# Kernel tuning notes

Hardware: AMD Instinct MI355X
Metric: run time of the kernel (lower is better)

Reference implementation:

```python
import jax, jax.numpy as jnp
import numpy as np

# ---- static module config (matches torch defaults) ----
N_LEVELS = 16
MIN_RES = 16
MAX_RES = 512
N_ENC = 2 ** 14
D = 3          # n_input_dims
E = 2          # n_embed_dims
B = 1 << 20    # number of query points

# per-level resolutions, computed in float32 to mirror torch's float32 log/exp
_gf = np.exp((np.log(np.float32(MAX_RES)) - np.log(np.float32(MIN_RES))) / np.float32(N_LEVELS - 1)).astype(np.float32)
RES = [int(np.floor(np.float32(MIN_RES) * _gf ** np.float32(l))) for l in range(N_LEVELS)]
DIRECT = [r ** D < N_ENC for r in RES]                  # small grids use direct ravel indexing
NLE = [min(r ** D, N_ENC) for r in RES]                  # encodings per level (sentinel row at index NLE[l])

# 2^D corner offsets, shape (8, 3)
OFFS = np.stack(np.meshgrid(*([np.arange(2)] * D), indexing='ij'), axis=-1).reshape(-1, D).astype(np.int32)
# instant-ngp spatial hashing primes
PRIMES = (1, 2654435761, 805459861)


def setup_inputs() -> dict:
    key = jax.random.key(0)
    k1, k2 = jax.random.split(key)
    x = jax.random.uniform(k1, (B, D), dtype=jnp.float32, minval=-1.0, maxval=1.0)
    # stacked per-level tables, padded to (N_ENC+1, E); rows >= NLE[l] zeroed
    emb = jax.random.uniform(k2, (N_LEVELS, N_ENC + 1, E), dtype=jnp.float32, minval=-1e-4, maxval=1e-4)
    row = np.arange(N_ENC + 1)
    valid = (row[None, :] < np.asarray(NLE)[:, None])    # (L, N_ENC+1); also zeroes the sentinel row
    emb = emb * jnp.asarray(valid[..., None], dtype=jnp.float32)
    return {"x": x, "emb": emb}


def _level_features(x, emb_l, R, n_encs, direct):
    offs = jnp.asarray(OFFS)                             # (8, 3)
    xs = (x + 1.0) * (R * 0.5) - 0.5                     # grid coords
    xl = jnp.floor(xs)
    frac = xs - xl                                       # (B, 3)
    xi = xl.astype(jnp.int32)
    c = xi[:, None, :] + offs[None, :, :]                # (B, 8, 3) corner indices
    # bilinear/trilinear weights: prod over dims of frac (offset=1) or 1-frac (offset=0)
    w = jnp.prod(jnp.where(offs[None].astype(bool), frac[:, None, :], 1.0 - frac[:, None, :]), axis=-1)  # (B, 8)
    w = jax.lax.stop_gradient(w)                         # torch computes weights under no_grad
    m = jnp.all((c >= 0) & (c < R), axis=-1)             # (B, 8) corner validity
    if direct:
        ids = (c[..., 0] * R + c[..., 1]) * R + c[..., 2]
    else:
        cu = c.astype(jnp.uint32)
        h = (cu[..., 0] * jnp.uint32(PRIMES[0])
             ^ cu[..., 1] * jnp.uint32(PRIMES[1])
             ^ cu[..., 2] * jnp.uint32(PRIMES[2]))
        ids = (h % jnp.uint32(n_encs)).astype(jnp.int32)
    ids = jnp.where(m, ids, n_encs)                      # invalid corners -> zero sentinel row
    return jnp.sum(emb_l[ids] * w[..., None], axis=1)    # (B, E)


def reference(x, emb):
    feats = [
        _level_features(x, emb[l], RES[l], NLE[l], DIRECT[l])
        for l in range(N_LEVELS)
    ]
    return jnp.stack(feats, axis=1)                      # (B, L, E)
```

## Files before the change

### kernel.cpp

```cpp
#include <hip/hip_runtime.h>


typedef __attribute__((ext_vector_type(2))) float f32x2;

#define B_POINTS (1 << 20)
#define N_LEVELS 16
#define TAB_F2   16385
#define WG       1024
#define NWG      512
#define NCHUNK   (NWG / N_LEVELS)
#define CHUNK    (B_POINTS / NCHUNK)
#define PPT      (CHUNK / WG)

__constant__ int   cRES[N_LEVELS]  = {16, 20, 25, 32, 40, 50, 64, 80,
                                      101, 128, 161, 203, 256, 322, 406, 512};
__constant__ float cHALF[N_LEVELS] = {8.f, 10.f, 12.5f, 16.f, 20.f, 25.f, 32.f, 40.f,
                                      50.5f, 64.f, 80.5f, 101.5f, 128.f, 161.f, 203.f, 256.f};

__global__ __launch_bounds__(WG)
void hashenc_lds(const float* __restrict__ x,
                 const float* __restrict__ emb,
                 float* __restrict__ out)
{
    __shared__ f32x2 tab[TAB_F2];

    const int bid = blockIdx.x;
    const int xcd = bid & 7;
    const int s   = bid >> 3;
    const int l   = s & 15;
    const int c   = ((s >> 4) << 3) | xcd;

    const int   R      = cRES[l];
    const float half   = cHALF[l];
    const bool  direct = (l < 3);

    const f32x2* __restrict__ gtab = (const f32x2*)emb + (size_t)l * TAB_F2;
    const int t = threadIdx.x;
#pragma unroll
    for (int j = 0; j < 16; ++j)
        tab[j * WG + t] = gtab[j * WG + t];
    if (t == 0) tab[16384] = gtab[16384];
    __syncthreads();

    const int base = c * CHUNK;
#pragma unroll 2
    for (int k = 0; k < PPT; ++k) {
        const int p = base + k * WG + t;

        const float x0 = x[p * 3 + 0];
        const float x1 = x[p * 3 + 1];
        const float x2 = x[p * 3 + 2];

        const float xs0 = (x0 + 1.0f) * half - 0.5f;
        const float xs1 = (x1 + 1.0f) * half - 0.5f;
        const float xs2 = (x2 + 1.0f) * half - 0.5f;
        const float fl0 = floorf(xs0), fl1 = floorf(xs1), fl2 = floorf(xs2);
        const float f0 = xs0 - fl0, f1 = xs1 - fl1, f2 = xs2 - fl2;
        const float g0 = 1.0f - f0, g1 = 1.0f - f1, g2 = 1.0f - f2;
        const int i0 = (int)fl0, i1 = (int)fl1, i2 = (int)fl2;

        const float wx0 = ((i0     >= 0) && (i0     < R)) ? g0 : 0.0f;
        const float wx1 = ((i0 + 1 >= 0) && (i0 + 1 < R)) ? f0 : 0.0f;
        const float wy0 = ((i1     >= 0) && (i1     < R)) ? g1 : 0.0f;
        const float wy1 = ((i1 + 1 >= 0) && (i1 + 1 < R)) ? f1 : 0.0f;
        const float wz0 = ((i2     >= 0) && (i2     < R)) ? g2 : 0.0f;
        const float wz1 = ((i2 + 1 >= 0) && (i2 + 1 < R)) ? f2 : 0.0f;

        const float pxy00 = wx0 * wy0, pxy01 = wx0 * wy1;
        const float pxy10 = wx1 * wy0, pxy11 = wx1 * wy1;
        const float w[8] = {pxy00 * wz0, pxy00 * wz1, pxy01 * wz0, pxy01 * wz1,
                            pxy10 * wz0, pxy10 * wz1, pxy11 * wz0, pxy11 * wz1};

        int id[8];
        if (direct) {
            const int Rm1 = R - 1;
            const int u0l = min(max(i0,     0), Rm1), u0h = min(max(i0 + 1, 0), Rm1);
            const int u1l = min(max(i1,     0), Rm1), u1h = min(max(i1 + 1, 0), Rm1);
            const int u2l = min(max(i2,     0), Rm1), u2h = min(max(i2 + 1, 0), Rm1);
            const int a0  = u0l * R, a1 = u0h * R;
            const int b00 = (a0 + u1l) * R, b01 = (a0 + u1h) * R;
            const int b10 = (a1 + u1l) * R, b11 = (a1 + u1h) * R;
            id[0] = b00 + u2l; id[1] = b00 + u2h; id[2] = b01 + u2l; id[3] = b01 + u2h;
            id[4] = b10 + u2l; id[5] = b10 + u2h; id[6] = b11 + u2l; id[7] = b11 + u2h;
        } else {
            const unsigned hx0 = (unsigned)i0,                   hx1 = (unsigned)(i0 + 1);
            const unsigned hy0 = (unsigned)i1 * 2654435761u,     hy1 = (unsigned)(i1 + 1) * 2654435761u;
            const unsigned hz0 = (unsigned)i2 * 805459861u,      hz1 = (unsigned)(i2 + 1) * 805459861u;
            id[0] = (int)((hx0 ^ hy0 ^ hz0) & 16383u); id[1] = (int)((hx0 ^ hy0 ^ hz1) & 16383u);
            id[2] = (int)((hx0 ^ hy1 ^ hz0) & 16383u); id[3] = (int)((hx0 ^ hy1 ^ hz1) & 16383u);
            id[4] = (int)((hx1 ^ hy0 ^ hz0) & 16383u); id[5] = (int)((hx1 ^ hy0 ^ hz1) & 16383u);
            id[6] = (int)((hx1 ^ hy1 ^ hz0) & 16383u); id[7] = (int)((hx1 ^ hy1 ^ hz1) & 16383u);
        }

        f32x2 acc = {0.0f, 0.0f};
#pragma unroll
        for (int q = 0; q < 8; ++q)
            acc += tab[id[q]] * w[q];

        ((f32x2*)out)[(size_t)p * N_LEVELS + l] = acc;
    }
}

extern "C" void kernel_launch(void* const* d_in, const int* in_sizes, int n_in,
                              void* d_out, int out_size, void* d_ws, size_t ws_size,
                              hipStream_t stream) {
    const float* x   = (const float*)d_in[0];
    const float* emb = (const float*)d_in[1];
    float* out = (float*)d_out;

    hashenc_lds<<<NWG, WG, 0, stream>>>(x, emb, out);
}
```

Baseline: 225.2 us.

## Prefetch point coordinates in groups and precompute byte offsets for LDS gathers

Halves the workgroup count so each block handles twice as many points per level. Coordinates for a group of four points are software-prefetched into registers, with the first group loaded before the table fill, which overlaps global loads with the LDS gathers. Address math is simplified: bounds checks are reduced to single comparisons, the scale uses a single FMA, and hash and direct indices are precomputed as byte offsets with the mask applied early. The trade-offs are fewer waves to hide latency, more register pressure, and a longer per-block tail.

```diff
diff --git a/kernel.cpp b/kernel.cpp
--- a/kernel.cpp
+++ b/kernel.cpp
@@ -7,10 +7,12 @@
 #define N_LEVELS 16
 #define TAB_F2   16385
 #define WG       1024
-#define NWG      512
+#define NWG      256
 #define NCHUNK   (NWG / N_LEVELS)
 #define CHUNK    (B_POINTS / NCHUNK)
 #define PPT      (CHUNK / WG)
+#define GRP      4
+#define NGRP     (PPT / GRP)
 
 __constant__ int   cRES[N_LEVELS]  = {16, 20, 25, 32, 40, 50, 64, 80,
                                       101, 128, 161, 203, 256, 322, 406, 512};
@@ -31,73 +33,105 @@
     const int c   = ((s >> 4) << 3) | xcd;
 
     const int   R      = cRES[l];
+    const int   Rm1    = R - 1;
     const float half   = cHALF[l];
+    const float hb     = half - 0.5f;
     const bool  direct = (l < 3);
+    const int   R8     = R * 8;
+    const int   RR8    = R * R * 8;
 
     const f32x2* __restrict__ gtab = (const f32x2*)emb + (size_t)l * TAB_F2;
-    const int t = threadIdx.x;
+    const int t    = threadIdx.x;
+    const int base = c * CHUNK + t;
+
+    float xa[GRP], xb[GRP], xcv[GRP];
+#pragma unroll
+    for (int j = 0; j < GRP; ++j) {
+        const int p = base + j * WG;
+        xa[j] = x[p * 3 + 0]; xb[j] = x[p * 3 + 1]; xcv[j] = x[p * 3 + 2];
+    }
+
 #pragma unroll
     for (int j = 0; j < 16; ++j)
         tab[j * WG + t] = gtab[j * WG + t];
     if (t == 0) tab[16384] = gtab[16384];
     __syncthreads();
 
-    const int base = c * CHUNK;
-#pragma unroll 2
-    for (int k = 0; k < PPT; ++k) {
-        const int p = base + k * WG + t;
+    const char* tb = (const char*)tab;
 
-        const float x0 = x[p * 3 + 0];
-        const float x1 = x[p * 3 + 1];
-        const float x2 = x[p * 3 + 2];
+    for (int kg = 0; kg < NGRP; ++kg) {
+        float ca[GRP], cb[GRP], cc[GRP];
+#pragma unroll
+        for (int j = 0; j < GRP; ++j) { ca[j] = xa[j]; cb[j] = xb[j]; cc[j] = xcv[j]; }
 
-        const float xs0 = (x0 + 1.0f) * half - 0.5f;
-        const float xs1 = (x1 + 1.0f) * half - 0.5f;
-        const float xs2 = (x2 + 1.0f) * half - 0.5f;
-        const float fl0 = floorf(xs0), fl1 = floorf(xs1), fl2 = floorf(xs2);
-        const float f0 = xs0 - fl0, f1 = xs1 - fl1, f2 = xs2 - fl2;
-        const float g0 = 1.0f - f0, g1 = 1.0f - f1, g2 = 1.0f - f2;
-        const int i0 = (int)fl0, i1 = (int)fl1, i2 = (int)fl2;
-
-        const float wx0 = ((i0     >= 0) && (i0     < R)) ? g0 : 0.0f;
-        const float wx1 = ((i0 + 1 >= 0) && (i0 + 1 < R)) ? f0 : 0.0f;
-        const float wy0 = ((i1     >= 0) && (i1     < R)) ? g1 : 0.0f;
-        const float wy1 = ((i1 + 1 >= 0) && (i1 + 1 < R)) ? f1 : 0.0f;
-        const float wz0 = ((i2     >= 0) && (i2     < R)) ? g2 : 0.0f;
-        const float wz1 = ((i2 + 1 >= 0) && (i2 + 1 < R)) ? f2 : 0.0f;
-
-        const float pxy00 = wx0 * wy0, pxy01 = wx0 * wy1;
-        const float pxy10 = wx1 * wy0, pxy11 = wx1 * wy1;
-        const float w[8] = {pxy00 * wz0, pxy00 * wz1, pxy01 * wz0, pxy01 * wz1,
-                            pxy10 * wz0, pxy10 * wz1, pxy11 * wz0, pxy11 * wz1};
-
-        int id[8];
-        if (direct) {
-            const int Rm1 = R - 1;
-            const int u0l = min(max(i0,     0), Rm1), u0h = min(max(i0 + 1, 0), Rm1);
-            const int u1l = min(max(i1,     0), Rm1), u1h = min(max(i1 + 1, 0), Rm1);
-            const int u2l = min(max(i2,     0), Rm1), u2h = min(max(i2 + 1, 0), Rm1);
-            const int a0  = u0l * R, a1 = u0h * R;
-            const int b00 = (a0 + u1l) * R, b01 = (a0 + u1h) * R;
-            const int b10 = (a1 + u1l) * R, b11 = (a1 + u1h) * R;
-            id[0] = b00 + u2l; id[1] = b00 + u2h; id[2] = b01 + u2l; id[3] = b01 + u2h;
-            id[4] = b10 + u2l; id[5] = b10 + u2h; id[6] = b11 + u2l; id[7] = b11 + u2h;
-        } else {
-            const unsigned hx0 = (unsigned)i0,                   hx1 = (unsigned)(i0 + 1);
-            const unsigned hy0 = (unsigned)i1 * 2654435761u,     hy1 = (unsigned)(i1 + 1) * 2654435761u;
-            const unsigned hz0 = (unsigned)i2 * 805459861u,      hz1 = (unsigned)(i2 + 1) * 805459861u;
-            id[0] = (int)((hx0 ^ hy0 ^ hz0) & 16383u); id[1] = (int)((hx0 ^ hy0 ^ hz1) & 16383u);
-            id[2] = (int)((hx0 ^ hy1 ^ hz0) & 16383u); id[3] = (int)((hx0 ^ hy1 ^ hz1) & 16383u);
-            id[4] = (int)((hx1 ^ hy0 ^ hz0) & 16383u); id[5] = (int)((hx1 ^ hy0 ^ hz1) & 16383u);
-            id[6] = (int)((hx1 ^ hy1 ^ hz0) & 16383u); id[7] = (int)((hx1 ^ hy1 ^ hz1) & 16383u);
+        if (kg + 1 < NGRP) {
+#pragma unroll
+            for (int j = 0; j < GRP; ++j) {
+                const int p = base + (kg + 1) * (GRP * WG) + j * WG;
+                xa[j] = x[p * 3 + 0]; xb[j] = x[p * 3 + 1]; xcv[j] = x[p * 3 + 2];
+            }
         }
 
-        f32x2 acc = {0.0f, 0.0f};
 #pragma unroll
-        for (int q = 0; q < 8; ++q)
-            acc += tab[id[q]] * w[q];
+        for (int j = 0; j < GRP; ++j) {
+            const int p = base + kg * (GRP * WG) + j * WG;
 
-        ((f32x2*)out)[(size_t)p * N_LEVELS + l] = acc;
+            const float xs0 = fmaf(ca[j], half, hb);
+            const float xs1 = fmaf(cb[j], half, hb);
+            const float xs2 = fmaf(cc[j], half, hb);
+            const float fl0 = floorf(xs0), fl1 = floorf(xs1), fl2 = floorf(xs2);
+            const float f0 = xs0 - fl0, f1 = xs1 - fl1, f2 = xs2 - fl2;
+            const float g0 = 1.0f - f0, g1 = 1.0f - f1, g2 = 1.0f - f2;
+            const int i0 = (int)fl0, i1 = (int)fl1, i2 = (int)fl2;
+
+            const float wx0 = (i0 >= 0)  ? g0 : 0.0f;
+            const float wx1 = (i0 < Rm1) ? f0 : 0.0f;
+            const float wy0 = (i1 >= 0)  ? g1 : 0.0f;
+            const float wy1 = (i1 < Rm1) ? f1 : 0.0f;
+            const float wz0 = (i2 >= 0)  ? g2 : 0.0f;
+            const float wz1 = (i2 < Rm1) ? f2 : 0.0f;
+
+            const float pxy00 = wx0 * wy0, pxy01 = wx0 * wy1;
+            const float pxy10 = wx1 * wy0, pxy11 = wx1 * wy1;
+            const float w0 = pxy00 * wz0, w1 = pxy00 * wz1;
+            const float w2 = pxy01 * wz0, w3 = pxy01 * wz1;
+            const float w4 = pxy10 * wz0, w5 = pxy10 * wz1;
+            const float w6 = pxy11 * wz0, w7 = pxy11 * wz1;
+
+            unsigned d0, d1, d2, d3, d4, d5, d6, d7;
+            if (direct) {
+                const int u0l = max(i0, 0), u0h = min(i0 + 1, Rm1);
+                const int u1l = max(i1, 0), u1h = min(i1 + 1, Rm1);
+                const int u2l = max(i2, 0), u2h = min(i2 + 1, Rm1);
+                const int a0  = u0l * RR8,     a1  = u0h * RR8;
+                const int b00 = a0 + u1l * R8, b01 = a0 + u1h * R8;
+                const int b10 = a1 + u1l * R8, b11 = a1 + u1h * R8;
+                const int zl  = u2l * 8,       zh  = u2h * 8;
+                d0 = b00 + zl; d1 = b00 + zh; d2 = b01 + zl; d3 = b01 + zh;
+                d4 = b10 + zl; d5 = b10 + zh; d6 = b11 + zl; d7 = b11 + zh;
+            } else {
+                const unsigned MB  = 16383u << 3;
+                const unsigned hx0 = (unsigned)i0 << 3,                 hx1 = hx0 + 8u;
+                const unsigned hy0 = (unsigned)i1 * (2654435761u * 8u), hy1 = hy0 + (2654435761u * 8u);
+                const unsigned hzf = (unsigned)i2 * (805459861u * 8u);
+                const unsigned hz0 = hzf & MB, hz1 = (hzf + (805459861u * 8u)) & MB;
+                const unsigned t00 = (hx0 ^ hy0) & MB, t01 = (hx0 ^ hy1) & MB;
+                const unsigned t10 = (hx1 ^ hy0) & MB, t11 = (hx1 ^ hy1) & MB;
+                d0 = t00 ^ hz0; d1 = t00 ^ hz1; d2 = t01 ^ hz0; d3 = t01 ^ hz1;
+                d4 = t10 ^ hz0; d5 = t10 ^ hz1; d6 = t11 ^ hz0; d7 = t11 ^ hz1;
+            }
+
+            f32x2 acc = *(const f32x2*)(tb + d0) * w0;
+            acc += *(const f32x2*)(tb + d1) * w1;
+            acc += *(const f32x2*)(tb + d2) * w2;
+            acc += *(const f32x2*)(tb + d3) * w3;
+            acc += *(const f32x2*)(tb + d4) * w4;
+            acc += *(const f32x2*)(tb + d5) * w5;
+            acc += *(const f32x2*)(tb + d6) * w6;
+            acc += *(const f32x2*)(tb + d7) * w7;
+
+            ((f32x2*)out)[(size_t)p * N_LEVELS + l] = acc;
+        }
     }
 }
 
```

After: 211.7 us. 6.0% less time.
